# Kernel tuning notes

Measured on AMD Instinct MI355X. Metric: run time of the kernel, lower is better.

The kernel has to match this reference:

```python
import jax, jax.numpy as jnp
import numpy as np

BS, T, N_AGENTS = 128, 256, 8
FEAT, MIX_EMB, EMB, HYP, STATE_DIM = 64, 32, 32, 256, 512


def setup_inputs() -> dict:
    key = jax.random.key(0)
    ks = jax.random.split(key, 30)
    s = 0.05
    inp = {
        "agent_qs": jax.random.normal(ks[0], (BS, T, N_AGENTS), jnp.float32),
        "hist": jax.random.normal(ks[1], (BS, T, N_AGENTS, MIX_EMB), jnp.float32),
        "states": jax.random.normal(ks[2], (BS, T, STATE_DIM), jnp.float32),
        "obs": jax.random.normal(ks[3], (BS, T, N_AGENTS, FEAT), jnp.float32),
        # token embedding + y_fc
        "W_tok": jax.random.normal(ks[4], (FEAT, MIX_EMB), jnp.float32) * s,
        "b_tok": jnp.zeros((MIX_EMB,), jnp.float32),
        "W_yfc": jax.random.normal(ks[5], (MIX_EMB, FEAT), jnp.float32) * s,
        "b_yfc": jnp.zeros((FEAT,), jnp.float32),
        # hyper_w_1: Linear(state,HYP)->ReLU->Linear(HYP, N_AGENTS*EMB)
        "W1a": jax.random.normal(ks[6], (STATE_DIM, HYP), jnp.float32) * s,
        "b1a": jnp.zeros((HYP,), jnp.float32),
        "W1b": jax.random.normal(ks[7], (HYP, N_AGENTS * EMB), jnp.float32) * s,
        "b1b": jnp.zeros((N_AGENTS * EMB,), jnp.float32),
        # hyper_w_final: Linear(state,HYP)->ReLU->Linear(HYP, EMB)
        "Wfa": jax.random.normal(ks[8], (STATE_DIM, HYP), jnp.float32) * s,
        "bfa": jnp.zeros((HYP,), jnp.float32),
        "Wfb": jax.random.normal(ks[9], (HYP, EMB), jnp.float32) * s,
        "bfb": jnp.zeros((EMB,), jnp.float32),
        # hyper_b_1
        "Wb1": jax.random.normal(ks[10], (STATE_DIM, EMB), jnp.float32) * s,
        "bb1": jnp.zeros((EMB,), jnp.float32),
        # V: Linear(state,EMB)->ReLU->Linear(EMB,1)
        "Wv1": jax.random.normal(ks[11], (STATE_DIM, EMB), jnp.float32) * s,
        "bv1": jnp.zeros((EMB,), jnp.float32),
        "Wv2": jax.random.normal(ks[12], (EMB, 1), jnp.float32) * s,
        "bv2": jnp.zeros((1,), jnp.float32),
    }
    return inp


def reference(agent_qs, hist, states, obs,
              W_tok, b_tok, W_yfc, b_yfc,
              W1a, b1a, W1b, b1b,
              Wfa, bfa, Wfb, bfb,
              Wb1, bb1, Wv1, bv1, Wv2, bv2):
    bs, t, _ = agent_qs.shape
    B = bs * t
    # (B, n_entities, feat); n_entities == n_agents here
    s = states.reshape(B, N_AGENTS, FEAT)
    e = jax.nn.relu(s @ W_tok + b_tok)            # token embedding
    y = e[:, :N_AGENTS]                            # transformer stand-in (identity)
    y = jax.nn.relu(y @ W_yfc + b_yfc).reshape(B, STATE_DIM)

    w1 = jnp.abs(jax.nn.relu(y @ W1a + b1a) @ W1b + b1b)
    w1 = w1.reshape(B, N_AGENTS, EMB)
    b1 = (y @ Wb1 + bb1)[:, None, :]               # (B,1,EMB)
    q = agent_qs.reshape(B, 1, N_AGENTS)
    hidden = jax.nn.elu(jnp.einsum('bia,bae->bie', q, w1) + b1)

    w_final = jnp.abs(jax.nn.relu(y @ Wfa + bfa) @ Wfb + bfb)  # (B,EMB)
    v = (jax.nn.relu(y @ Wv1 + bv1) @ Wv2 + bv2)               # (B,1)
    q_tot = (jnp.einsum('bie,be->bi', hidden, w_final) + v).reshape(bs, t, 1)

    # gradient branch (agent_qs detached in original; no-op in fwd-only)
    hidden2 = jax.nn.elu(jnp.einsum('bia,bae->bie', q, w1) + b1)[:, 0, :]
    delu = jnp.where(hidden2 < 0, jnp.exp(hidden2), jnp.ones_like(hidden2))
    # bmm(w1, diag(delu)) @ w_final == einsum over elementwise-scaled w1
    grad = jnp.einsum('bae,be,be->ba', w1, delu, w_final).reshape(bs, t, N_AGENTS)
    return q_tot, grad
```

## Files before the change

kernel.cpp:

```cpp
#include <hip/hip_runtime.h>
#include <math.h>


#define NB 32768
#define TB 64
#define THREADS 512
#define NBLOCKS (NB / TB)

typedef short sh8 __attribute__((ext_vector_type(8)));
typedef float f4 __attribute__((ext_vector_type(4)));
typedef unsigned short ush;

#define OFF_WCAT_H 0
#define OFF_WCAT_L 327680
#define OFF_W1B_H  655360
#define OFF_W1B_L  720896
#define OFF_WFB_H  786432
#define OFF_WFB_L  794624
#define OFF_TOK_H  802816
#define OFF_TOK_L  804864
#define OFF_YFC_H  806912
#define OFF_YFC_L  808960

__device__ __forceinline__ ush f2bf(float x) {
    unsigned u = __float_as_uint(x);
    u += 0x7fffu + ((u >> 16) & 1u);
    return (ush)(u >> 16);
}
__device__ __forceinline__ float bf2f(ush h) {
    return __uint_as_float(((unsigned)h) << 16);
}
__device__ __forceinline__ void splitbf(float x, ush& h, ush& l) {
    h = f2bf(x);
    l = f2bf(x - bf2f(h));
}
__device__ __forceinline__ f4 mfma(sh8 a, sh8 b, f4 c) {
    return __builtin_amdgcn_mfma_f32_16x16x32_bf16(a, b, c, 0, 0, 0);
}

__device__ __forceinline__ unsigned swY(unsigned a) {
    return a ^ (((((a >> 10) & 7) ^ ((a >> 7) & 7)) << 4));
}
__device__ __forceinline__ unsigned swH(unsigned a) {
    return a ^ (((a >> 9) & 7) << 4);
}
__device__ __forceinline__ unsigned swS(unsigned a) {
    return a ^ (((a >> 7) & 3) << 4);
}

__device__ void tileFrag(const float* src, int snc, int scol0, int ncol, int nk,
                         ush* dH, ush* dL, int nkcg, int tg0, int kcg0,
                         float (*T)[68])
{
    const int tid = threadIdx.x;
    const int nc4 = ncol >> 2;
    const int s_r = (nc4 == 16) ? 4 : 3;
    for (int i = tid; i < nk * nc4; i += 256) {
        const int r = i >> s_r, c4 = i & (nc4 - 1);
        const float4 v = *(const float4*)(src + (size_t)r * snc + scol0 + c4 * 4);
        T[r][c4 * 4 + 0] = v.x; T[r][c4 * 4 + 1] = v.y;
        T[r][c4 * 4 + 2] = v.z; T[r][c4 * 4 + 3] = v.w;
    }
    __syncthreads();
    const int nkc = nk >> 5;
    const int nfrag = (ncol >> 4) * nkc;
    const int l = tid & 63, l16 = l & 15, lq = l >> 4;
    for (int f = tid >> 6; f < nfrag; f += 4) {
        const int tl = f / nkc, kl = f % nkc;
        ush hv[8], lv[8];
        #pragma unroll
        for (int j = 0; j < 8; j++) {
            const float x = T[kl * 32 + lq * 8 + j][tl * 16 + l16];
            ush h, lo; splitbf(x, h, lo);
            hv[j] = h; lv[j] = lo;
        }
        const size_t a = (size_t)(((tg0 + tl) * nkcg + (kcg0 + kl)) * 64 + l) * 8;
        uint4 H, L;
        H.x = (unsigned)hv[0] | ((unsigned)hv[1] << 16);
        H.y = (unsigned)hv[2] | ((unsigned)hv[3] << 16);
        H.z = (unsigned)hv[4] | ((unsigned)hv[5] << 16);
        H.w = (unsigned)hv[6] | ((unsigned)hv[7] << 16);
        L.x = (unsigned)lv[0] | ((unsigned)lv[1] << 16);
        L.y = (unsigned)lv[2] | ((unsigned)lv[3] << 16);
        L.z = (unsigned)lv[4] | ((unsigned)lv[5] << 16);
        L.w = (unsigned)lv[6] | ((unsigned)lv[7] << 16);
        *(uint4*)(dH + a) = H;
        *(uint4*)(dL + a) = L;
    }
    __syncthreads();
}

__global__ __launch_bounds__(256) void xmix_prep(
    const float* __restrict__ W_tok, const float* __restrict__ W_yfc,
    const float* __restrict__ W1a, const float* __restrict__ W1b,
    const float* __restrict__ Wfa, const float* __restrict__ Wfb,
    const float* __restrict__ Wb1, const float* __restrict__ Wv1,
    ush* __restrict__ ws)
{
    __shared__ float T[64][68];
    const int b = blockIdx.x;
    if (b < 80) {
        const int kt = b / 10, ct = b % 10;
        const int k0 = kt * 64, kcg0 = kt * 2;
        if (ct < 4) {
            tileFrag(W1a + (size_t)k0 * 256, 256, ct * 64, 64, 64,
                     ws + OFF_WCAT_H, ws + OFF_WCAT_L, 16, ct * 4, kcg0, T);
        } else if (ct < 8) {
            tileFrag(Wfa + (size_t)k0 * 256, 256, (ct - 4) * 64, 64, 64,
                     ws + OFF_WCAT_H, ws + OFF_WCAT_L, 16, 16 + (ct - 4) * 4, kcg0, T);
        } else if (ct == 8) {
            tileFrag(Wb1 + (size_t)k0 * 32, 32, 0, 32, 64,
                     ws + OFF_WCAT_H, ws + OFF_WCAT_L, 16, 32, kcg0, T);
            tileFrag(Wv1 + (size_t)k0 * 32, 32, 0, 32, 64,
                     ws + OFF_WCAT_H, ws + OFF_WCAT_L, 16, 34, kcg0, T);
        } else {
            const int l = threadIdx.x & 63;
            const uint4 z = {0, 0, 0, 0};
            for (int f = threadIdx.x >> 6; f < 8; f += 4) {
                const int tl = f >> 1, kl = f & 1;
                const size_t a = (size_t)(((36 + tl) * 16 + (kcg0 + kl)) * 64 + l) * 8;
                *(uint4*)(ws + OFF_WCAT_H + a) = z;
                *(uint4*)(ws + OFF_WCAT_L + a) = z;
            }
        }
    } else if (b < 96) {
        const int i = b - 80, kt = i >> 2, ct = i & 3;
        tileFrag(W1b + (size_t)(kt * 64) * 256, 256, ct * 64, 64, 64,
                 ws + OFF_W1B_H, ws + OFF_W1B_L, 8, ct * 4, kt * 2, T);
    } else if (b < 100) {
        const int kt = b - 96;
        tileFrag(Wfb + (size_t)(kt * 64) * 32, 32, 0, 32, 64,
                 ws + OFF_WFB_H, ws + OFF_WFB_L, 8, 0, kt * 2, T);
    } else if (b == 100) {
        tileFrag(W_tok, 32, 0, 32, 64, ws + OFF_TOK_H, ws + OFF_TOK_L, 2, 0, 0, T);
    } else {
        tileFrag(W_yfc, 64, 0, 64, 32, ws + OFF_YFC_H, ws + OFF_YFC_L, 1, 0, 0, T);
    }
}

__global__ __launch_bounds__(THREADS, 2) void xmix_mfma(
    const float* __restrict__ agent_qs,
    const float* __restrict__ states,
    const ush* __restrict__ ws,
    const float* __restrict__ b_tok, const float* __restrict__ b_yfc,
    const float* __restrict__ b1a,  const float* __restrict__ b1b,
    const float* __restrict__ bfa,  const float* __restrict__ bfb,
    const float* __restrict__ bb1,  const float* __restrict__ bv1,
    const float* __restrict__ Wv2,  const float* __restrict__ bv2,
    float* __restrict__ out)
{
    __shared__ __align__(16) unsigned char BBs[131072];
    __shared__ __align__(16) unsigned char SMs[16384];

    const int tid = threadIdx.x;
    const int wv = tid >> 6;
    const int l   = tid & 63;
    const int l16 = l & 15;
    const int lq  = l >> 4;
    const int base = blockIdx.x * TB;
    const f4 fzero = {0.f, 0.f, 0.f, 0.f};

    {
        const float4* gs = (const float4*)(states + (size_t)base * 512);
        #pragma unroll
        for (int i = 0; i < 16; i++) {
            const int idx4 = tid + THREADS * i;
            const float4 v = gs[idx4];
            const int e0 = idx4 * 4;
            const int s = e0 >> 9, c = e0 & 511;
            ush h0, h1, h2, h3, q0, q1, q2, q3;
            splitbf(v.x, h0, q0); splitbf(v.y, h1, q1);
            splitbf(v.z, h2, q2); splitbf(v.w, h3, q3);
            const unsigned sa = swY((unsigned)(s * 1024 + c * 2));
            uint2 uh, ul;
            uh.x = (unsigned)h0 | ((unsigned)h1 << 16);
            uh.y = (unsigned)h2 | ((unsigned)h3 << 16);
            ul.x = (unsigned)q0 | ((unsigned)q1 << 16);
            ul.y = (unsigned)q2 | ((unsigned)q3 << 16);
            *(uint2*)(&BBs[sa])         = uh;
            *(uint2*)(&BBs[65536 + sa]) = ul;
        }
    }
    __syncthreads();

    {
        const ush* tokH = ws + OFF_TOK_H;
        const ush* tokL = ws + OFF_TOK_L;
        const ush* yfcH = ws + OFF_YFC_H;
        const ush* yfcL = ws + OFF_YFC_L;
        unsigned char* scr = &SMs[wv * 2048];

        float btok[2];
        btok[0] = b_tok[l16]; btok[1] = b_tok[16 + l16];
        float byfc[4];
        #pragma unroll
        for (int n = 0; n < 4; n++) byfc[n] = b_yfc[n * 16 + l16];

        sh8 TBh[2][2], TBl[2][2];
        #pragma unroll
        for (int n = 0; n < 2; n++)
            #pragma unroll
            for (int kc = 0; kc < 2; kc++) {
                const int fo = ((n * 2 + kc) * 64 + l) * 8;
                TBh[n][kc] = *(const sh8*)(tokH + fo);
                TBl[n][kc] = *(const sh8*)(tokL + fo);
            }
        sh8 YBh[4], YBl[4];
        #pragma unroll
        for (int n = 0; n < 4; n++) {
            const int fo = (n * 64 + l) * 8;
            YBh[n] = *(const sh8*)(yfcH + fo);
            YBl[n] = *(const sh8*)(yfcL + fo);
        }

        #pragma unroll
        for (int i = 0; i < 4; i++) {
            const int rt = wv * 4 + i;
            const int r = rt * 16 + l16;
            const int s = r >> 3, a = r & 7;
            f4 eacc[2] = {fzero, fzero};
            #pragma unroll
            for (int kc = 0; kc < 2; kc++) {
                const unsigned ad = (unsigned)(s * 1024 + (a * 64 + kc * 32 + lq * 8) * 2);
                const unsigned sa = swY(ad);
                const sh8 Ah = *(const sh8*)(&BBs[sa]);
                const sh8 Al = *(const sh8*)(&BBs[65536 + sa]);
                #pragma unroll
                for (int n = 0; n < 2; n++) {
                    eacc[n] = mfma(Ah, TBh[n][kc], eacc[n]);
                    eacc[n] = mfma(Ah, TBl[n][kc], eacc[n]);
                    eacc[n] = mfma(Al, TBh[n][kc], eacc[n]);
                }
            }
            #pragma unroll
            for (int n = 0; n < 2; n++)
                #pragma unroll
                for (int j = 0; j < 4; j++) {
                    const float e = fmaxf(eacc[n][j] + btok[n], 0.f);
                    const unsigned sa = swS((unsigned)((lq * 4 + j) * 64 + (n * 16 + l16) * 2));
                    ush hh, ll; splitbf(e, hh, ll);
                    *(ush*)(scr + sa)        = hh;
                    *(ush*)(scr + 1024 + sa) = ll;
                }
            f4 yacc[4] = {fzero, fzero, fzero, fzero};
            {
                const unsigned sa = swS((unsigned)(l16 * 64 + lq * 16));
                const sh8 Ah = *(const sh8*)(scr + sa);
                const sh8 Al = *(const sh8*)(scr + 1024 + sa);
                #pragma unroll
                for (int n = 0; n < 4; n++) {
                    yacc[n] = mfma(Ah, YBh[n], yacc[n]);
                    yacc[n] = mfma(Ah, YBl[n], yacc[n]);
                    yacc[n] = mfma(Al, YBh[n], yacc[n]);
                }
            }
            #pragma unroll
            for (int n = 0; n < 4; n++)
                #pragma unroll
                for (int j = 0; j < 4; j++) {
                    const float y = fmaxf(yacc[n][j] + byfc[n], 0.f);
                    const int rr = rt * 16 + lq * 4 + j;
                    const int ss = rr >> 3, aa = rr & 7, ff = n * 16 + l16;
                    const unsigned sa = swY((unsigned)(ss * 1024 + (aa * 64 + ff) * 2));
                    ush hh, ll; splitbf(y, hh, ll);
                    *(ush*)(&BBs[sa])         = hh;
                    *(ush*)(&BBs[65536 + sa]) = ll;
                }
        }
    }
    __syncthreads();

    f4 acc3[4][5];
    #pragma unroll
    for (int m = 0; m < 4; m++)
        #pragma unroll
        for (int t = 0; t < 5; t++) acc3[m][t] = fzero;
    {
        const ush* wcH = ws + OFF_WCAT_H;
        const ush* wcL = ws + OFF_WCAT_L;
        int cb[5];
        #pragma unroll
        for (int t = 0; t < 5; t++) cb[t] = (wv * 5 + t) * 8192;
        int rowb[4];
        #pragma unroll
        for (int m = 0; m < 4; m++) rowb[m] = (m * 16 + l16) * 1024;

        sh8 BhA[5], BlA[5], BhB[5], BlB[5];

#define LOADB(BH, BL, KC) { const int fo_ = (KC) * 512 + l * 8; \
        _Pragma("unroll") \
        for (int t = 0; t < 5; t++) { \
            BH[t] = *(const sh8*)(wcH + cb[t] + fo_); \
            BL[t] = *(const sh8*)(wcL + cb[t] + fo_); \
        } }

#define DOMFMA(BH, BL, KC) { \
        const int ko_ = (KC) * 32 + lq * 8; \
        sh8 Ah_[4], Al_[4]; \
        _Pragma("unroll") \
        for (int m = 0; m < 4; m++) { \
            const unsigned sa_ = swY((unsigned)(rowb[m] + ko_ * 2)); \
            Ah_[m] = *(const sh8*)(&BBs[sa_]); \
            Al_[m] = *(const sh8*)(&BBs[65536 + sa_]); \
        } \
        _Pragma("unroll") \
        for (int m = 0; m < 4; m++) \
            _Pragma("unroll") \
            for (int t = 0; t < 5; t++) acc3[m][t] = mfma(Ah_[m], BH[t], acc3[m][t]); \
        _Pragma("unroll") \
        for (int m = 0; m < 4; m++) \
            _Pragma("unroll") \
            for (int t = 0; t < 5; t++) acc3[m][t] = mfma(Ah_[m], BL[t], acc3[m][t]); \
        _Pragma("unroll") \
        for (int m = 0; m < 4; m++) \
            _Pragma("unroll") \
            for (int t = 0; t < 5; t++) acc3[m][t] = mfma(Al_[m], BH[t], acc3[m][t]); \
        }

        LOADB(BhA, BlA, 0);
        #pragma unroll 1
        for (int kc2 = 0; kc2 < 8; kc2++) {
            LOADB(BhB, BlB, kc2 * 2 + 1);
            DOMFMA(BhA, BlA, kc2 * 2);
            LOADB(BhA, BlA, kc2 * 2 + 2);
            DOMFMA(BhB, BlB, kc2 * 2 + 1);
        }
#undef LOADB
#undef DOMFMA
    }
    __syncthreads();

    {
        #pragma unroll
        for (int t = 0; t < 5; t++) {
            const int gt = wv * 5 + t;
            const int cg = gt * 16 + l16;
            if (gt < 16) {
                const float bias = b1a[cg];
                #pragma unroll
                for (int m = 0; m < 4; m++)
                    #pragma unroll
                    for (int j = 0; j < 4; j++) {
                        const int row = m * 16 + lq * 4 + j;
                        const float h = fmaxf(acc3[m][t][j] + bias, 0.f);
                        ush hh, ll; splitbf(h, hh, ll);
                        const unsigned sa = swH((unsigned)(row * 512 + cg * 2));
                        *(ush*)(&BBs[sa])         = hh;
                        *(ush*)(&BBs[32768 + sa]) = ll;
                    }
            } else if (gt < 32) {
                const int c = cg - 256;
                const float bias = bfa[c];
                #pragma unroll
                for (int m = 0; m < 4; m++)
                    #pragma unroll
                    for (int j = 0; j < 4; j++) {
                        const int row = m * 16 + lq * 4 + j;
                        const float h = fmaxf(acc3[m][t][j] + bias, 0.f);
                        ush hh, ll; splitbf(h, hh, ll);
                        const unsigned sa = swH((unsigned)(row * 512 + c * 2));
                        *(ush*)(&BBs[65536 + sa]) = hh;
                        *(ush*)(&BBs[98304 + sa]) = ll;
                    }
            } else if (gt < 34) {
                const int c = cg - 512;
                const float bias = bb1[c];
                #pragma unroll
                for (int m = 0; m < 4; m++)
                    #pragma unroll
                    for (int j = 0; j < 4; j++) {
                        const int row = m * 16 + lq * 4 + j;
                        *(float*)(&SMs[(row * 32 + c) * 4]) = acc3[m][t][j] + bias;
                    }
            } else if (gt < 36) {
                const int c = cg - 544;
                const float bias = bv1[c];
                #pragma unroll
                for (int m = 0; m < 4; m++)
                    #pragma unroll
                    for (int j = 0; j < 4; j++) {
                        const int row = m * 16 + lq * 4 + j;
                        *(float*)(&SMs[8192 + (row * 32 + c) * 4]) =
                            fmaxf(acc3[m][t][j] + bias, 0.f);
                    }
            }
        }
    }
    __syncthreads();

    f4 acc4[4][2];
    #pragma unroll
    for (int m = 0; m < 4; m++) { acc4[m][0] = fzero; acc4[m][1] = fzero; }
    f4 accw = fzero;
    {
        const ush* w1H = ws + OFF_W1B_H;
        const ush* w1L = ws + OFF_W1B_L;
        const ush* wfH = ws + OFF_WFB_H;
        const ush* wfL = ws + OFF_WFB_L;
        const int mw = wv & 3, nw = wv >> 2;
        const int cb0 = (wv * 2 + 0) * 4096;
        const int cb1 = (wv * 2 + 1) * 4096;
        const int cbw = nw * 4096;
        #pragma unroll 2
        for (int kc = 0; kc < 8; kc++) {
            const int fo = kc * 512 + l * 8;
            const int ko = kc * 32 + lq * 8;
            const sh8 B0h = *(const sh8*)(w1H + cb0 + fo);
            const sh8 B0l = *(const sh8*)(w1L + cb0 + fo);
            const sh8 B1h = *(const sh8*)(w1H + cb1 + fo);
            const sh8 B1l = *(const sh8*)(w1L + cb1 + fo);
            const sh8 Wh  = *(const sh8*)(wfH + cbw + fo);
            const sh8 Wl  = *(const sh8*)(wfL + cbw + fo);
            sh8 Ah[4], Al[4];
            #pragma unroll
            for (int m = 0; m < 4; m++) {
                const unsigned sa = swH((unsigned)((m * 16 + l16) * 512 + ko * 2));
                Ah[m] = *(const sh8*)(&BBs[sa]);
                Al[m] = *(const sh8*)(&BBs[32768 + sa]);
            }
            const unsigned saw = swH((unsigned)((mw * 16 + l16) * 512 + ko * 2));
            const sh8 Awh = *(const sh8*)(&BBs[65536 + saw]);
            const sh8 Awl = *(const sh8*)(&BBs[98304 + saw]);
            #pragma unroll
            for (int m = 0; m < 4; m++) {
                acc4[m][0] = mfma(Ah[m], B0h, acc4[m][0]);
                acc4[m][1] = mfma(Ah[m], B1h, acc4[m][1]);
            }
            accw = mfma(Awh, Wh, accw);
            #pragma unroll
            for (int m = 0; m < 4; m++) {
                acc4[m][0] = mfma(Ah[m], B0l, acc4[m][0]);
                acc4[m][1] = mfma(Ah[m], B1l, acc4[m][1]);
            }
            accw = mfma(Awh, Wl, accw);
            #pragma unroll
            for (int m = 0; m < 4; m++) {
                acc4[m][0] = mfma(Al[m], B0h, acc4[m][0]);
                acc4[m][1] = mfma(Al[m], B1h, acc4[m][1]);
            }
            accw = mfma(Awl, Wh, accw);
        }
    }
    __syncthreads();

    {
        #pragma unroll
        for (int t = 0; t < 2; t++) {
            const int col = (wv * 2 + t) * 16 + l16;
            const int a = col >> 5, e = col & 31;
            const float bias = b1b[col];
            #pragma unroll
            for (int m = 0; m < 4; m++)
                #pragma unroll
                for (int j = 0; j < 4; j++) {
                    const int row = m * 16 + lq * 4 + j;
                    *(float*)(&BBs[(row * 264 + a * 33 + e) * 4]) =
                        fabsf(acc4[m][t][j] + bias);
                }
        }
        {
            const int mw = wv & 3, nw = wv >> 2;
            const int col = nw * 16 + l16;
            const float bias = bfb[col];
            #pragma unroll
            for (int j = 0; j < 4; j++) {
                const int row = mw * 16 + lq * 4 + j;
                *(float*)(&BBs[67584 + (row * 33 + col) * 4]) =
                    fabsf(accw[j] + bias);
            }
        }
    }
    __syncthreads();

    {
        const int s = tid >> 3, li = tid & 7;
        const int b = base + s;
        float q[8];
        #pragma unroll
        for (int a = 0; a < 8; a++) q[a] = agent_qs[(size_t)b * 8 + a];
        const float* w1p = (const float*)(&BBs[0]);
        const float* wfp = (const float*)(&BBs[67584]);
        const float* b1p = (const float*)(&SMs[0]);
        float* hidp = (float*)(&BBs[76032]);
        float* tpp  = (float*)(&BBs[84480]);
        #pragma unroll
        for (int ii = 0; ii < 4; ii++) {
            const int e = li + 8 * ii;
            float z = b1p[s * 32 + e];
            #pragma unroll
            for (int a = 0; a < 8; a++) z = fmaf(q[a], w1p[s * 264 + a * 33 + e], z);
            const float h = (z > 0.f) ? z : (expf(z) - 1.f);
            const float d = (h < 0.f) ? expf(h) : 1.f;
            hidp[s * 33 + e] = h;
            tpp[s * 33 + e] = d * wfp[s * 33 + e];
        }
    }
    __syncthreads();
    {
        const float* w1p = (const float*)(&BBs[0]);
        const float* wfp = (const float*)(&BBs[67584]);
        const float* v1p = (const float*)(&SMs[8192]);
        const float* hidp = (const float*)(&BBs[76032]);
        const float* tpp  = (const float*)(&BBs[84480]);
        {
            const int s = tid >> 3, a = tid & 7;
            const int b = base + s;
            float g = 0.f;
            #pragma unroll
            for (int e = 0; e < 32; e++)
                g = fmaf(w1p[s * 264 + a * 33 + e], tpp[s * 33 + e], g);
            out[NB + (size_t)b * 8 + a] = g;
        }
        if (tid < 64) {
            const int s2 = tid, b2 = base + s2;
            float v = bv2[0];
            #pragma unroll
            for (int e = 0; e < 32; e++) v = fmaf(v1p[s2 * 32 + e], Wv2[e], v);
            float qt = v;
            #pragma unroll
            for (int e = 0; e < 32; e++)
                qt = fmaf(hidp[s2 * 33 + e], wfp[s2 * 33 + e], qt);
            out[b2] = qt;
        }
    }
}

extern "C" void kernel_launch(void* const* d_in, const int* in_sizes, int n_in,
                              void* d_out, int out_size, void* d_ws, size_t ws_size,
                              hipStream_t stream) {
    const float* agent_qs = (const float*)d_in[0];
    const float* states   = (const float*)d_in[2];
    const float* W_tok = (const float*)d_in[4];
    const float* b_tok = (const float*)d_in[5];
    const float* W_yfc = (const float*)d_in[6];
    const float* b_yfc = (const float*)d_in[7];
    const float* W1a   = (const float*)d_in[8];
    const float* b1a   = (const float*)d_in[9];
    const float* W1b   = (const float*)d_in[10];
    const float* b1b   = (const float*)d_in[11];
    const float* Wfa   = (const float*)d_in[12];
    const float* bfa   = (const float*)d_in[13];
    const float* Wfb   = (const float*)d_in[14];
    const float* bfb   = (const float*)d_in[15];
    const float* Wb1   = (const float*)d_in[16];
    const float* bb1   = (const float*)d_in[17];
    const float* Wv1   = (const float*)d_in[18];
    const float* bv1   = (const float*)d_in[19];
    const float* Wv2   = (const float*)d_in[20];
    const float* bv2   = (const float*)d_in[21];
    float* out = (float*)d_out;
    ush* ws = (ush*)d_ws;

    xmix_prep<<<102, 256, 0, stream>>>(W_tok, W_yfc, W1a, W1b, Wfa, Wfb, Wb1, Wv1, ws);
    xmix_mfma<<<NBLOCKS, THREADS, 0, stream>>>(
        agent_qs, states, ws, b_tok, b_yfc, b1a, b1b, bfa, bfb,
        bb1, bv1, Wv2, bv2, out);
}
```

Baseline: 264.7 us.

## Load states directly into MFMA fragments and drop padded zero tiles

Removes the up-front staging of the whole states tile into LDS as split bf16, and instead loads each row's float4s from global memory directly into registers and splits them just before the token-embedding MFMA. The concatenated hidden-layer GEMM stops computing the four all-zero padding column tiles: waves 0-3 take five tiles and waves 4-7 take four. The prep kernel gives Wv1 its own block. Together these cut one barrier, the LDS staging traffic and wasted MFMAs. In exchange, the scattered global loads in the first stage may coalesce less well, and the uneven tile split across waves adds control divergence.

```diff
diff --git a/kernel.cpp b/kernel.cpp
--- a/kernel.cpp
+++ b/kernel.cpp
@@ -36,6 +36,17 @@
 }
 __device__ __forceinline__ f4 mfma(sh8 a, sh8 b, f4 c) {
     return __builtin_amdgcn_mfma_f32_16x16x32_bf16(a, b, c, 0, 0, 0);
+}
+__device__ __forceinline__ void split8(const float4 v0, const float4 v1, sh8& Ah, sh8& Al) {
+    ush h, l;
+    splitbf(v0.x, h, l); Ah[0] = (short)h; Al[0] = (short)l;
+    splitbf(v0.y, h, l); Ah[1] = (short)h; Al[1] = (short)l;
+    splitbf(v0.z, h, l); Ah[2] = (short)h; Al[2] = (short)l;
+    splitbf(v0.w, h, l); Ah[3] = (short)h; Al[3] = (short)l;
+    splitbf(v1.x, h, l); Ah[4] = (short)h; Al[4] = (short)l;
+    splitbf(v1.y, h, l); Ah[5] = (short)h; Al[5] = (short)l;
+    splitbf(v1.z, h, l); Ah[6] = (short)h; Al[6] = (short)l;
+    splitbf(v1.w, h, l); Ah[7] = (short)h; Al[7] = (short)l;
 }
 
 __device__ __forceinline__ unsigned swY(unsigned a) {
@@ -99,8 +110,8 @@
 {
     __shared__ float T[64][68];
     const int b = blockIdx.x;
-    if (b < 80) {
-        const int kt = b / 10, ct = b % 10;
+    if (b < 88) {
+        const int kt = b / 11, ct = b % 11;
         const int k0 = kt * 64, kcg0 = kt * 2;
         if (ct < 4) {
             tileFrag(W1a + (size_t)k0 * 256, 256, ct * 64, 64, 64,
@@ -111,6 +122,7 @@
         } else if (ct == 8) {
             tileFrag(Wb1 + (size_t)k0 * 32, 32, 0, 32, 64,
                      ws + OFF_WCAT_H, ws + OFF_WCAT_L, 16, 32, kcg0, T);
+        } else if (ct == 9) {
             tileFrag(Wv1 + (size_t)k0 * 32, 32, 0, 32, 64,
                      ws + OFF_WCAT_H, ws + OFF_WCAT_L, 16, 34, kcg0, T);
         } else {
@@ -123,15 +135,15 @@
                 *(uint4*)(ws + OFF_WCAT_L + a) = z;
             }
         }
-    } else if (b < 96) {
-        const int i = b - 80, kt = i >> 2, ct = i & 3;
+    } else if (b < 104) {
+        const int i = b - 88, kt = i >> 2, ct = i & 3;
         tileFrag(W1b + (size_t)(kt * 64) * 256, 256, ct * 64, 64, 64,
                  ws + OFF_W1B_H, ws + OFF_W1B_L, 8, ct * 4, kt * 2, T);
-    } else if (b < 100) {
-        const int kt = b - 96;
+    } else if (b < 108) {
+        const int kt = b - 104;
         tileFrag(Wfb + (size_t)(kt * 64) * 32, 32, 0, 32, 64,
                  ws + OFF_WFB_H, ws + OFF_WFB_L, 8, 0, kt * 2, T);
-    } else if (b == 100) {
+    } else if (b == 108) {
         tileFrag(W_tok, 32, 0, 32, 64, ws + OFF_TOK_H, ws + OFF_TOK_L, 2, 0, 0, T);
     } else {
         tileFrag(W_yfc, 64, 0, 64, 32, ws + OFF_YFC_H, ws + OFF_YFC_L, 1, 0, 0, T);
@@ -161,29 +173,6 @@
     const f4 fzero = {0.f, 0.f, 0.f, 0.f};
 
     {
-        const float4* gs = (const float4*)(states + (size_t)base * 512);
-        #pragma unroll
-        for (int i = 0; i < 16; i++) {
-            const int idx4 = tid + THREADS * i;
-            const float4 v = gs[idx4];
-            const int e0 = idx4 * 4;
-            const int s = e0 >> 9, c = e0 & 511;
-            ush h0, h1, h2, h3, q0, q1, q2, q3;
-            splitbf(v.x, h0, q0); splitbf(v.y, h1, q1);
-            splitbf(v.z, h2, q2); splitbf(v.w, h3, q3);
-            const unsigned sa = swY((unsigned)(s * 1024 + c * 2));
-            uint2 uh, ul;
-            uh.x = (unsigned)h0 | ((unsigned)h1 << 16);
-            uh.y = (unsigned)h2 | ((unsigned)h3 << 16);
-            ul.x = (unsigned)q0 | ((unsigned)q1 << 16);
-            ul.y = (unsigned)q2 | ((unsigned)q3 << 16);
-            *(uint2*)(&BBs[sa])         = uh;
-            *(uint2*)(&BBs[65536 + sa]) = ul;
-        }
-    }
-    __syncthreads();
-
-    {
         const ush* tokH = ws + OFF_TOK_H;
         const ush* tokL = ws + OFF_TOK_L;
         const ush* yfcH = ws + OFF_YFC_H;
@@ -217,14 +206,14 @@
         for (int i = 0; i < 4; i++) {
             const int rt = wv * 4 + i;
             const int r = rt * 16 + l16;
-            const int s = r >> 3, a = r & 7;
+            const float* srow = states + (size_t)(base + (r >> 3)) * 512 + (r & 7) * 64;
             f4 eacc[2] = {fzero, fzero};
             #pragma unroll
             for (int kc = 0; kc < 2; kc++) {
-                const unsigned ad = (unsigned)(s * 1024 + (a * 64 + kc * 32 + lq * 8) * 2);
-                const unsigned sa = swY(ad);
-                const sh8 Ah = *(const sh8*)(&BBs[sa]);
-                const sh8 Al = *(const sh8*)(&BBs[65536 + sa]);
+                const float4 v0 = *(const float4*)(srow + kc * 32 + lq * 8);
+                const float4 v1 = *(const float4*)(srow + kc * 32 + lq * 8 + 4);
+                sh8 Ah, Al;
+                split8(v0, v1, Ah, Al);
                 #pragma unroll
                 for (int n = 0; n < 2; n++) {
                     eacc[n] = mfma(Ah, TBh[n][kc], eacc[n]);
@@ -268,124 +257,148 @@
                 }
         }
     }
-    __syncthreads();
 
     f4 acc3[4][5];
     #pragma unroll
     for (int m = 0; m < 4; m++)
         #pragma unroll
         for (int t = 0; t < 5; t++) acc3[m][t] = fzero;
-    {
-        const ush* wcH = ws + OFF_WCAT_H;
-        const ush* wcL = ws + OFF_WCAT_L;
-        int cb[5];
-        #pragma unroll
-        for (int t = 0; t < 5; t++) cb[t] = (wv * 5 + t) * 8192;
-        int rowb[4];
-        #pragma unroll
-        for (int m = 0; m < 4; m++) rowb[m] = (m * 16 + l16) * 1024;
-
-        sh8 BhA[5], BlA[5], BhB[5], BlB[5];
-
-#define LOADB(BH, BL, KC) { const int fo_ = (KC) * 512 + l * 8; \
-        _Pragma("unroll") \
-        for (int t = 0; t < 5; t++) { \
-            BH[t] = *(const sh8*)(wcH + cb[t] + fo_); \
-            BL[t] = *(const sh8*)(wcL + cb[t] + fo_); \
-        } }
-
-#define DOMFMA(BH, BL, KC) { \
-        const int ko_ = (KC) * 32 + lq * 8; \
-        sh8 Ah_[4], Al_[4]; \
-        _Pragma("unroll") \
-        for (int m = 0; m < 4; m++) { \
-            const unsigned sa_ = swY((unsigned)(rowb[m] + ko_ * 2)); \
-            Ah_[m] = *(const sh8*)(&BBs[sa_]); \
-            Al_[m] = *(const sh8*)(&BBs[65536 + sa_]); \
-        } \
+
+    const ush* wcH = ws + OFF_WCAT_H;
+    const ush* wcL = ws + OFF_WCAT_L;
+    const int tb0 = (wv < 4) ? (wv * 5) : (20 + (wv - 4) * 4);
+    int cb[5];
+    #pragma unroll
+    for (int t = 0; t < 5; t++) cb[t] = (tb0 + t) * 8192;
+    int rowb[4];
+    #pragma unroll
+    for (int m = 0; m < 4; m++) rowb[m] = (m * 16 + l16) * 1024;
+
+    sh8 BhA[5], BlA[5], BhB[5], BlB[5];
+
+#define LOADB(BH, BL, KC, N) { const int fo_ = (KC) * 512 + l * 8; \
+    _Pragma("unroll") \
+    for (int t = 0; t < N; t++) { \
+        BH[t] = *(const sh8*)(wcH + cb[t] + fo_); \
+        BL[t] = *(const sh8*)(wcL + cb[t] + fo_); \
+    } }
+
+#define DOMFMA(BH, BL, KC, N) { \
+    const int ko_ = (KC) * 32 + lq * 8; \
+    sh8 Ah_[4], Al_[4]; \
+    _Pragma("unroll") \
+    for (int m = 0; m < 4; m++) { \
+        const unsigned sa_ = swY((unsigned)(rowb[m] + ko_ * 2)); \
+        Ah_[m] = *(const sh8*)(&BBs[sa_]); \
+        Al_[m] = *(const sh8*)(&BBs[65536 + sa_]); \
+    } \
+    _Pragma("unroll") \
+    for (int m = 0; m < 4; m++) \
+        _Pragma("unroll") \
+        for (int t = 0; t < N; t++) acc3[m][t] = mfma(Ah_[m], BH[t], acc3[m][t]); \
+    _Pragma("unroll") \
+    for (int m = 0; m < 4; m++) \
+        _Pragma("unroll") \
+        for (int t = 0; t < N; t++) acc3[m][t] = mfma(Ah_[m], BL[t], acc3[m][t]); \
+    _Pragma("unroll") \
+    for (int m = 0; m < 4; m++) \
+        _Pragma("unroll") \
+        for (int t = 0; t < N; t++) acc3[m][t] = mfma(Al_[m], BH[t], acc3[m][t]); \
+    }
+
+    if (wv < 4) { LOADB(BhA, BlA, 0, 5); } else { LOADB(BhA, BlA, 0, 4); }
+    __syncthreads();
+
+    if (wv < 4) {
+        #pragma unroll 1
+        for (int kc2 = 0; kc2 < 8; kc2++) {
+            LOADB(BhB, BlB, kc2 * 2 + 1, 5);
+            DOMFMA(BhA, BlA, kc2 * 2, 5);
+            LOADB(BhA, BlA, kc2 * 2 + 2, 5);
+            DOMFMA(BhB, BlB, kc2 * 2 + 1, 5);
+        }
+    } else {
+        #pragma unroll 1
+        for (int kc2 = 0; kc2 < 8; kc2++) {
+            LOADB(BhB, BlB, kc2 * 2 + 1, 4);
+            DOMFMA(BhA, BlA, kc2 * 2, 4);
+            LOADB(BhA, BlA, kc2 * 2 + 2, 4);
+            DOMFMA(BhB, BlB, kc2 * 2 + 1, 4);
+        }
+    }
+#undef LOADB
+#undef DOMFMA
+
+    const ush* w1H = ws + OFF_W1B_H;
+    const ush* w1L = ws + OFF_W1B_L;
+    const ush* wfH = ws + OFF_WFB_H;
+    const ush* wfL = ws + OFF_WFB_L;
+    const int mw = wv & 3, nw = wv >> 2;
+    const int cb0 = (wv * 2 + 0) * 4096;
+    const int cb1 = (wv * 2 + 1) * 4096;
+    const int cbw = nw * 4096;
+
+    __syncthreads();
+
+#define EPIBODY(T_) { \
+    const int gt = tb0 + (T_); \
+    const int cg = gt * 16 + l16; \
+    if (gt < 16) { \
+        const float bias = b1a[cg]; \
         _Pragma("unroll") \
         for (int m = 0; m < 4; m++) \
             _Pragma("unroll") \
-            for (int t = 0; t < 5; t++) acc3[m][t] = mfma(Ah_[m], BH[t], acc3[m][t]); \
+            for (int j = 0; j < 4; j++) { \
+                const int row = m * 16 + lq * 4 + j; \
+                const float h = fmaxf(acc3[m][T_][j] + bias, 0.f); \
+                ush hh, ll; splitbf(h, hh, ll); \
+                const unsigned sa = swH((unsigned)(row * 512 + cg * 2)); \
+                *(ush*)(&BBs[sa])         = hh; \
+                *(ush*)(&BBs[32768 + sa]) = ll; \
+            } \
+    } else if (gt < 32) { \
+        const int c = cg - 256; \
+        const float bias = bfa[c]; \
         _Pragma("unroll") \
         for (int m = 0; m < 4; m++) \
             _Pragma("unroll") \
-            for (int t = 0; t < 5; t++) acc3[m][t] = mfma(Ah_[m], BL[t], acc3[m][t]); \
+            for (int j = 0; j < 4; j++) { \
+                const int row = m * 16 + lq * 4 + j; \
+                const float h = fmaxf(acc3[m][T_][j] + bias, 0.f); \
+                ush hh, ll; splitbf(h, hh, ll); \
+                const unsigned sa = swH((unsigned)(row * 512 + c * 2)); \
+                *(ush*)(&BBs[65536 + sa]) = hh; \
+                *(ush*)(&BBs[98304 + sa]) = ll; \
+            } \
+    } else if (gt < 34) { \
+        const int c = cg - 512; \
+        const float bias = bb1[c]; \
         _Pragma("unroll") \
         for (int m = 0; m < 4; m++) \
             _Pragma("unroll") \
-            for (int t = 0; t < 5; t++) acc3[m][t] = mfma(Al_[m], BH[t], acc3[m][t]); \
-        }
-
-        LOADB(BhA, BlA, 0);
-        #pragma unroll 1
-        for (int kc2 = 0; kc2 < 8; kc2++) {
-            LOADB(BhB, BlB, kc2 * 2 + 1);
-            DOMFMA(BhA, BlA, kc2 * 2);
-            LOADB(BhA, BlA, kc2 * 2 + 2);
-            DOMFMA(BhB, BlB, kc2 * 2 + 1);
-        }
-#undef LOADB
-#undef DOMFMA
-    }
-    __syncthreads();
-
-    {
-        #pragma unroll
-        for (int t = 0; t < 5; t++) {
-            const int gt = wv * 5 + t;
-            const int cg = gt * 16 + l16;
-            if (gt < 16) {
-                const float bias = b1a[cg];
-                #pragma unroll
-                for (int m = 0; m < 4; m++)
-                    #pragma unroll
-                    for (int j = 0; j < 4; j++) {
-                        const int row = m * 16 + lq * 4 + j;
-                        const float h = fmaxf(acc3[m][t][j] + bias, 0.f);
-                        ush hh, ll; splitbf(h, hh, ll);
-                        const unsigned sa = swH((unsigned)(row * 512 + cg * 2));
-                        *(ush*)(&BBs[sa])         = hh;
-                        *(ush*)(&BBs[32768 + sa]) = ll;
-                    }
-            } else if (gt < 32) {
-                const int c = cg - 256;
-                const float bias = bfa[c];
-                #pragma unroll
-                for (int m = 0; m < 4; m++)
-                    #pragma unroll
-                    for (int j = 0; j < 4; j++) {
-                        const int row = m * 16 + lq * 4 + j;
-                        const float h = fmaxf(acc3[m][t][j] + bias, 0.f);
-                        ush hh, ll; splitbf(h, hh, ll);
-                        const unsigned sa = swH((unsigned)(row * 512 + c * 2));
-                        *(ush*)(&BBs[65536 + sa]) = hh;
-                        *(ush*)(&BBs[98304 + sa]) = ll;
-                    }
-            } else if (gt < 34) {
-                const int c = cg - 512;
-                const float bias = bb1[c];
-                #pragma unroll
-                for (int m = 0; m < 4; m++)
-                    #pragma unroll
-                    for (int j = 0; j < 4; j++) {
-                        const int row = m * 16 + lq * 4 + j;
-                        *(float*)(&SMs[(row * 32 + c) * 4]) = acc3[m][t][j] + bias;
-                    }
-            } else if (gt < 36) {
-                const int c = cg - 544;
-                const float bias = bv1[c];
-                #pragma unroll
-                for (int m = 0; m < 4; m++)
-                    #pragma unroll
-                    for (int j = 0; j < 4; j++) {
-                        const int row = m * 16 + lq * 4 + j;
-                        *(float*)(&SMs[8192 + (row * 32 + c) * 4]) =
-                            fmaxf(acc3[m][t][j] + bias, 0.f);
-                    }
-            }
-        }
-    }
+            for (int j = 0; j < 4; j++) { \
+                const int row = m * 16 + lq * 4 + j; \
+                *(float*)(&SMs[(row * 32 + c) * 4]) = acc3[m][T_][j] + bias; \
+            } \
+    } else if (gt < 36) { \
+        const int c = cg - 544; \
+        const float bias = bv1[c]; \
+        _Pragma("unroll") \
+        for (int m = 0; m < 4; m++) \
+            _Pragma("unroll") \
+            for (int j = 0; j < 4; j++) { \
+                const int row = m * 16 + lq * 4 + j; \
+                *(float*)(&SMs[8192 + (row * 32 + c) * 4]) = \
+                    fmaxf(acc3[m][T_][j] + bias, 0.f); \
+            } \
+    } }
+
+    if (wv < 4) {
+        EPIBODY(0) EPIBODY(1) EPIBODY(2) EPIBODY(3) EPIBODY(4)
+    } else {
+        EPIBODY(0) EPIBODY(1) EPIBODY(2) EPIBODY(3)
+    }
+#undef EPIBODY
     __syncthreads();
 
     f4 acc4[4][2];
@@ -393,14 +406,6 @@
     for (int m = 0; m < 4; m++) { acc4[m][0] = fzero; acc4[m][1] = fzero; }
     f4 accw = fzero;
     {
-        const ush* w1H = ws + OFF_W1B_H;
-        const ush* w1L = ws + OFF_W1B_L;
-        const ush* wfH = ws + OFF_WFB_H;
-        const ush* wfL = ws + OFF_WFB_L;
-        const int mw = wv & 3, nw = wv >> 2;
-        const int cb0 = (wv * 2 + 0) * 4096;
-        const int cb1 = (wv * 2 + 1) * 4096;
-        const int cbw = nw * 4096;
         #pragma unroll 2
         for (int kc = 0; kc < 8; kc++) {
             const int fo = kc * 512 + l * 8;
@@ -459,7 +464,6 @@
                 }
         }
         {
-            const int mw = wv & 3, nw = wv >> 2;
             const int col = nw * 16 + l16;
             const float bias = bfb[col];
             #pragma unroll
@@ -551,7 +555,7 @@
     float* out = (float*)d_out;
     ush* ws = (ush*)d_ws;
 
-    xmix_prep<<<102, 256, 0, stream>>>(W_tok, W_yfc, W1a, W1b, Wfa, Wfb, Wb1, Wv1, ws);
+    xmix_prep<<<110, 256, 0, stream>>>(W_tok, W_yfc, W1a, W1b, Wfa, Wfb, Wb1, Wv1, ws);
     xmix_mfma<<<NBLOCKS, THREADS, 0, stream>>>(
         agent_qs, states, ws, b_tok, b_yfc, b1a, b1b, bfa, bfb,
         bb1, bv1, Wv2, bv2, out);
```

Result: faster. 250.2 us (-5.5%).
